# Kernel optimization log

Hardware: AMD Instinct MI355X
Metric: run time of the kernel (lower is better)

Reference implementation:

```python
import jax, jax.numpy as jnp
import numpy as np

B, L, D, H = 2, 2048, 1024, 16
HD = D // H
ROPE_BASE = 10000.0


def _chain_info(lengths):
    """lengths: [B, L] int, chain lengths packed at the front, zeros after.
    Returns per-position within-chain positions (RoPE resets per chain),
    chain ids, and a validity mask."""
    def one(row):
        csum = jnp.cumsum(row)                      # [L]
        total = csum[-1]
        p = jnp.arange(L)
        cid = jnp.searchsorted(csum, p, side='right')  # chain id per position
        prev = jnp.where(cid > 0, csum[jnp.clip(cid - 1, 0, L - 1)], 0)
        valid = p < total
        pos = jnp.where(valid, p - prev, 0).astype(jnp.float32)
        return pos, cid, valid
    return jax.vmap(one)(lengths)


def _rope_tables(pos):
    # pos: [B, L] float -> cos/sin [B, L, 1, HD]
    inv_freq = 1.0 / (ROPE_BASE ** (jnp.arange(0, HD, 2, dtype=jnp.float32) / HD))
    freqs = pos[..., None] * inv_freq               # [B, L, HD/2]
    emb = jnp.concatenate([freqs, freqs], axis=-1)  # [B, L, HD]
    return jnp.cos(emb)[:, :, None, :], jnp.sin(emb)[:, :, None, :]


def _apply_rope(x, cos, sin):
    d = x.shape[-1]
    x1, x2 = x[..., : d // 2], x[..., d // 2:]
    return x * cos + jnp.concatenate([-x2, x1], axis=-1) * sin


def _branch(x, Wqkv, bqkv, cos, sin, allowed):
    # x: [B, L, D]; allowed: [B, L, L] bool attention mask for this branch
    qkv = x @ Wqkv.T + bqkv                          # [B, L, 3D]
    qkv = qkv.reshape(B, L, 3, H, HD)
    q, k, v = qkv[:, :, 0], qkv[:, :, 1], qkv[:, :, 2]
    q = q * (HD ** -0.5)
    q = _apply_rope(q, cos, sin)
    k = _apply_rope(k, cos, sin)
    scores = jnp.einsum('bthd,bshd->bhts', q, k)     # [B, H, L, L]
    scores = jnp.where(allowed[:, None], scores, -jnp.inf)
    probs = jax.nn.softmax(scores, axis=-1)
    probs = jnp.where(jnp.isnan(probs), 0.0, probs)  # fully-masked rows -> 0
    out = jnp.einsum('bhts,bshd->bthd', probs, v)    # [B, L, H, HD]
    return out.reshape(B, L, D)


def setup_inputs() -> dict:
    key = jax.random.key(0)
    ks = jax.random.split(key, 7)
    s = 0.02
    lens = np.zeros((B, L), np.int64)
    lens[0, :8] = [300, 250, 200, 400, 350, 248, 150, 100]   # sum 1998
    lens[1, :6] = [512, 400, 300, 360, 276, 200]             # sum 2048
    return {
        'hidden_states': jax.random.normal(ks[0], (B, L, D), jnp.float32),
        'attention_mask_in_length': jnp.asarray(lens),
        'Wqkv_intra': jax.random.normal(ks[1], (3 * D, D), jnp.float32) * s,
        'bqkv_intra': jnp.zeros((3 * D,), jnp.float32),
        'Wqkv_inter': jax.random.normal(ks[2], (3 * D, D), jnp.float32) * s,
        'bqkv_inter': jnp.zeros((3 * D,), jnp.float32),
        'Wout': jax.random.normal(ks[3], (D, D), jnp.float32) * s,
        'bout': jnp.zeros((D,), jnp.float32),
    }


def reference(hidden_states, attention_mask_in_length, Wqkv_intra, bqkv_intra,
              Wqkv_inter, bqkv_inter, Wout, bout):
    pos, cid, valid = _chain_info(attention_mask_in_length)
    cos, sin = _rope_tables(pos)
    same_chain = cid[:, :, None] == cid[:, None, :]          # [B, L, L]
    key_valid = valid[:, None, :]                            # [B, 1, L]
    allowed_intra = same_chain & key_valid
    allowed_inter = (~same_chain) & key_valid
    out_intra = _branch(hidden_states, Wqkv_intra, bqkv_intra, cos, sin, allowed_intra)
    out_inter = _branch(hidden_states, Wqkv_inter, bqkv_inter, cos, sin, allowed_inter)
    return (out_intra + out_inter) @ Wout.T + bout
```

## Files before the change

kernel.cpp:

```cpp
#include <hip/hip_runtime.h>
#include <hip/hip_bf16.h>
#include <stdint.h>

#define B 2
#define L 2048
#define D 1024
#define H 16
#define HD 64
#define NT (L / 64)
#define NQT (L / 128)
#define INVALID_CID 0x40000000

typedef __hip_bfloat16 bf16;
typedef __attribute__((ext_vector_type(8))) short short8;
typedef __attribute__((ext_vector_type(4))) float floatx4;
typedef __attribute__((ext_vector_type(4))) unsigned int uint4v;

static __device__ __forceinline__ short f2bf(float f) {
    bf16 h = __float2bfloat16(f);
    return *reinterpret_cast<short*>(&h);
}

static __device__ __forceinline__ void async_copy16(const void* g, void* l) {
    __builtin_amdgcn_global_load_lds((__attribute__((address_space(1))) void*)g,
                                     (__attribute__((address_space(3))) void*)l,
                                     16, 0, 0);
}

__global__ void chain_kernel(const int* __restrict__ lens,
                             float* __restrict__ pos, int* __restrict__ cid,
                             int4* __restrict__ tinfo)
{
    __shared__ int csum[L];
    __shared__ int cids[L];
    __shared__ int part[256];
    int b = blockIdx.x;
    int t = threadIdx.x;

    int loc[8];
    int s = 0;
    #pragma unroll
    for (int j = 0; j < 8; ++j) { s += lens[b * L + t * 8 + j]; loc[j] = s; }
    part[t] = s;
    __syncthreads();
    if (t == 0) {
        int acc = 0;
        for (int i = 0; i < 256; ++i) { int v = part[i]; part[i] = acc; acc += v; }
    }
    __syncthreads();
    int base = part[t];
    #pragma unroll
    for (int j = 0; j < 8; ++j) csum[t * 8 + j] = base + loc[j];
    __syncthreads();

    int total = csum[L - 1];
    for (int p = t; p < L; p += 256) {
        int cv;
        if (p < total) {
            int lo = 0, hi = L;
            while (lo < hi) {
                int mid = (lo + hi) >> 1;
                if (csum[mid] <= p) lo = mid + 1; else hi = mid;
            }
            int prev = (lo > 0) ? csum[lo - 1] : 0;
            pos[b * L + p] = (float)(p - prev);
            cv = lo;
        } else {
            pos[b * L + p] = 0.f;
            cv = INVALID_CID;
        }
        cids[p] = cv;
        cid[b * L + p] = cv;
    }
    __syncthreads();
    if (t < NT) {
        int mn = 0x7fffffff, mx = -1, any = 0, all = 1;
        for (int j = 0; j < 64; ++j) {
            int cv = cids[t * 64 + j];
            if (cv != INVALID_CID) { any = 1; mn = min(mn, cv); mx = max(mx, cv); }
            else all = 0;
        }
        tinfo[b * NT + t] = make_int4(mn, mx, any | (all << 1), 0);
    }
}

__global__ void cast_all(const float* __restrict__ x,  const float* __restrict__ Wi,
                         const float* __restrict__ We, const float* __restrict__ Wo,
                         bf16* __restrict__ xb, bf16* __restrict__ Wib,
                         bf16* __restrict__ Web, bf16* __restrict__ Wob)
{
    int bid = blockIdx.x;
    const float* src; bf16* dst; int base;
    if      (bid < 4096)  { src = x;  dst = xb;  base = bid; }
    else if (bid < 7168)  { src = Wi; dst = Wib; base = bid - 4096; }
    else if (bid < 10240) { src = We; dst = Web; base = bid - 7168; }
    else                  { src = Wo; dst = Wob; base = bid - 10240; }
    int i = (base * 256 + threadIdx.x) * 4;
    float4 v = *(const float4*)(src + i);
    dst[i + 0] = __float2bfloat16(v.x);
    dst[i + 1] = __float2bfloat16(v.y);
    dst[i + 2] = __float2bfloat16(v.z);
    dst[i + 3] = __float2bfloat16(v.w);
}

__global__ __launch_bounds__(256, 4) void gemm128(
    const bf16* __restrict__ A, const bf16* __restrict__ Bw,
    const float* __restrict__ bias, const float* __restrict__ bias2,
    void* __restrict__ Cout, int M, int N, int K, int c_bf16, int nsplit)
{
    __shared__ short As[128 * 32];
    __shared__ short Bs[128 * 32];

    int tid = threadIdx.x;
    int wave = tid >> 6, lane = tid & 63;
    int i15 = lane & 15, q8 = lane >> 4;
    int wm = wave & 1, wn = wave >> 1;
    int m0 = blockIdx.y * 128, n0 = blockIdx.x * 128;

    floatx4 acc[4][4];
    #pragma unroll
    for (int mt = 0; mt < 4; ++mt)
        #pragma unroll
        for (int nt = 0; nt < 4; ++nt) acc[mt][nt] = (floatx4){0.f, 0.f, 0.f, 0.f};

    const short* gA = (const short*)A  + (size_t)(m0 + wave * 32 + (lane >> 2)) * K + (lane & 3) * 8;
    const short* gB = (const short*)Bw + (size_t)(n0 + wave * 32 + (lane >> 2)) * K + (lane & 3) * 8;
    short* lA = As + wave * 1024;
    short* lB = Bs + wave * 1024;

    for (int kt = 0; kt < K; kt += 32) {
        __syncthreads();
        async_copy16(gA + kt,          lA);
        async_copy16(gA + 16 * K + kt, lA + 512);
        async_copy16(gB + kt,          lB);
        async_copy16(gB + 16 * K + kt, lB + 512);
        __syncthreads();

        short8 af[4], bfr[4];
        #pragma unroll
        for (int mt = 0; mt < 4; ++mt)
            af[mt] = *(const short8*)&As[(wm * 64 + mt * 16 + i15) * 32 + q8 * 8];
        #pragma unroll
        for (int nt = 0; nt < 4; ++nt)
            bfr[nt] = *(const short8*)&Bs[(wn * 64 + nt * 16 + i15) * 32 + q8 * 8];
        #pragma unroll
        for (int mt = 0; mt < 4; ++mt)
            #pragma unroll
            for (int nt = 0; nt < 4; ++nt)
                acc[mt][nt] = __builtin_amdgcn_mfma_f32_16x16x32_bf16(af[mt], bfr[nt], acc[mt][nt], 0, 0, 0);
    }

    #pragma unroll
    for (int nt = 0; nt < 4; ++nt) {
        int n = n0 + wn * 64 + nt * 16 + i15;
        float bv = (n < nsplit) ? bias[n] : bias2[n - nsplit];
        #pragma unroll
        for (int mt = 0; mt < 4; ++mt) {
            #pragma unroll
            for (int rg = 0; rg < 4; ++rg) {
                int m = m0 + wm * 64 + mt * 16 + q8 * 4 + rg;
                float v = acc[mt][nt][rg] + bv;
                if (c_bf16) ((bf16*)Cout)[(size_t)m * N + n] = __float2bfloat16(v);
                else        ((float*)Cout)[(size_t)m * N + n] = v;
            }
        }
    }
}

__global__ __launch_bounds__(256) void rope_scatter2(
    const bf16* __restrict__ qkv, int rowstride, const float* __restrict__ pos,
    bf16* __restrict__ Qo, bf16* __restrict__ Ko, bf16* __restrict__ Vtg)
{
    __shared__ float Vsh[64][65];
    int tid = threadIdx.x;
    int bid = blockIdx.x;
    int lt = bid & (NT - 1);
    int h  = (bid >> 5) & (H - 1);
    int b  = bid >> 9;
    int l0 = lt * 64;

    const float QSCALE = 0.18033688011111772f;
    int hd = tid & 63, lq = tid >> 6;
    float sgn = (hd < 32) ? -1.f : 1.f;
    float invf = exp2f(-(float)(hd & 31) * (13.287712379549449f / 32.f));

    #pragma unroll
    for (int rr = 0; rr < 16; ++rr) {
        int l = l0 + lq * 16 + rr;
        size_t row = (size_t)(b * L + l) * rowstride;
        int col  = h * HD + hd;
        int col2 = h * HD + (hd ^ 32);

        float xq  = __bfloat162float(qkv[row + col]);
        float xq2 = __bfloat162float(qkv[row + col2]);
        float xk  = __bfloat162float(qkv[row + D + col]);
        float xk2 = __bfloat162float(qkv[row + D + col2]);
        float xv  = __bfloat162float(qkv[row + 2 * D + col]);

        float p = pos[b * L + l];
        float ang = p * invf;
        float cc = cosf(ang), ss = sinf(ang);

        float qo = QSCALE * (xq * cc + sgn * xq2 * ss);
        float ko = xk * cc + sgn * xk2 * ss;

        size_t o = ((size_t)(b * H + h) * L + l) * HD + hd;
        Qo[o] = __float2bfloat16(qo);
        Ko[o] = __float2bfloat16(ko);
        Vsh[l - l0][hd] = xv;
    }
    __syncthreads();
    int lcol = tid & 63, dq = tid >> 6;
    #pragma unroll
    for (int rr = 0; rr < 16; ++rr) {
        int dd = dq * 16 + rr;
        Vtg[((size_t)(b * H + h) * HD + dd) * L + l0 + lcol] = __float2bfloat16(Vsh[lcol][dd]);
    }
}

__global__ __launch_bounds__(256, 2) void attn6(
    const bf16* __restrict__ Q, const bf16* __restrict__ Kg, const bf16* __restrict__ Vtg,
    const int* __restrict__ cid, const int4* __restrict__ tinfo,
    float* __restrict__ OutF, bf16* __restrict__ OutB, const float* __restrict__ Prev,
    int branch)
{
    __shared__ short Ks[2][64][72];
    __shared__ short Vs[2][64][72];
    __shared__ int cls_s[NT];
    __shared__ int list_s[NT];
    __shared__ int nlist_s;

    int tid = threadIdx.x;
    int wave = tid >> 6, lane = tid & 63;
    int i15 = lane & 15, q8 = lane >> 4;
    int workid = ((blockIdx.x & 7) << 6) | (blockIdx.x >> 3);
    int qt = workid & (NQT - 1);
    int h  = (workid >> 4) & (H - 1);
    int b  = workid >> 8;
    int q0 = qt * 128;
    const size_t bh  = (size_t)(b * H + h) * L;
    const size_t bhd = (size_t)(b * H + h) * HD;

    short8 qf[2][2];
    int cq[2];
    #pragma unroll
    for (int g = 0; g < 2; ++g) {
        const short* qp = (const short*)Q + (bh + q0 + g * 64 + wave * 16 + i15) * HD + q8 * 8;
        qf[g][0] = *(const short8*)(qp);
        qf[g][1] = *(const short8*)(qp + 32);
        cq[g] = cid[b * L + q0 + g * 64 + wave * 16 + i15];
    }

    int4 qa = tinfo[b * NT + 2 * qt];
    int4 qb4 = tinfo[b * NT + 2 * qt + 1];
    int4 qinf;
    qinf.x = min(qa.x, qb4.x);
    qinf.y = max(qa.y, qb4.y);
    qinf.z = ((qa.z | qb4.z) & 1) | (qa.z & qb4.z & 2);
    int qall = (qinf.z >> 1) & 1;

    if (tid < NT) {
        int4 ki = tinfo[b * NT + tid];
        int kany = ki.z & 1, kall = (ki.z >> 1) & 1;
        bool disjoint = (ki.x > qinf.y) || (ki.y < qinf.x);
        bool mono = qall && kall && (qinf.x == qinf.y) && (ki.x == ki.y) && (qinf.x == ki.x);
        int cls;
        if (branch == 0) {
            if (!kany || disjoint) cls = 0;
            else if (mono) cls = 2;
            else cls = 1;
        } else {
            if (!kany || mono) cls = 0;
            else if (kall && disjoint) cls = 2;
            else cls = 1;
        }
        cls_s[tid] = cls;
    }
    __syncthreads();
    if (tid == 0) {
        int n = 0;
        for (int t = 0; t < NT; ++t) {
            int c = cls_s[t];
            if (c) list_s[n++] = (t * 64) | ((c == 2) << 16);
        }
        nlist_s = n;
    }
    __syncthreads();
    int n = nlist_s;

    int r = tid >> 2, ccol = (tid & 3) * 16;
    int sr = ((((r >> 2) & 1) | ((r >> 5) << 1)) << 4) | (((r >> 3) & 3) << 2) | (r & 3);
    const short* Kbase = (const short*)Kg  + (bh + r) * HD + ccol;
    const short* Vbase = (const short*)Vtg + (bhd + r) * L + ccol;

    int4 pk0, pk1, pv0, pv1;
    int cur = 0;
    if (n > 0) {
        cur = list_s[0];
        int kt0 = cur & 0xffff;
        pk0 = *(const int4*)(Kbase + (size_t)kt0 * HD);
        pk1 = *(const int4*)(Kbase + (size_t)kt0 * HD + 8);
        pv0 = *(const int4*)(Vbase + kt0);
        pv1 = *(const int4*)(Vbase + kt0 + 8);
    }

    floatx4 accO[2][4];
    #pragma unroll
    for (int g = 0; g < 2; ++g)
        #pragma unroll
        for (int t = 0; t < 4; ++t) accO[g][t] = (floatx4){0.f, 0.f, 0.f, 0.f};
    float lsum[2] = {0.f, 0.f};

    for (int i = 0; i < n; ++i) {
        int kt = cur & 0xffff, full = cur >> 16;
        int buf = i & 1;

        *(int4*)&Ks[buf][sr][ccol]     = pk0;
        *(int4*)&Ks[buf][sr][ccol + 8] = pk1;
        *(int4*)&Vs[buf][r][ccol]      = pv0;
        *(int4*)&Vs[buf][r][ccol + 8]  = pv1;
        __syncthreads();

        if (i + 1 < n) {
            cur = list_s[i + 1];
            int nk = cur & 0xffff;
            pk0 = *(const int4*)(Kbase + (size_t)nk * HD);
            pk1 = *(const int4*)(Kbase + (size_t)nk * HD + 8);
            pv0 = *(const int4*)(Vbase + nk);
            pv1 = *(const int4*)(Vbase + nk + 8);
        }

        unsigned int dl[2][4], dh[2][4];
        #pragma unroll
        for (int t = 0; t < 4; ++t) {
            short8 b0 = *(const short8*)&Ks[buf][t * 16 + i15][q8 * 8];
            short8 b1 = *(const short8*)&Ks[buf][t * 16 + i15][32 + q8 * 8];

            floatx4 accS[2];
            #pragma unroll
            for (int g = 0; g < 2; ++g) {
                accS[g] = (floatx4){0.f, 0.f, 0.f, 0.f};
                accS[g] = __builtin_amdgcn_mfma_f32_16x16x32_bf16(b0, qf[g][0], accS[g], 0, 0, 0);
                accS[g] = __builtin_amdgcn_mfma_f32_16x16x32_bf16(b1, qf[g][1], accS[g], 0, 0, 0);
            }

            if (!full) {
                int4 ck4 = *(const int4*)(cid + b * L + kt + (q8 << 3) + ((t & 1) << 2) + ((t >> 1) << 5));
                int ckr[4] = {ck4.x, ck4.y, ck4.z, ck4.w};
                #pragma unroll
                for (int g = 0; g < 2; ++g)
                    #pragma unroll
                    for (int rg = 0; rg < 4; ++rg) {
                        bool kv = (ckr[rg] != INVALID_CID);
                        bool match = (cq[g] == ckr[rg]);
                        bool ok = kv && (branch ? !match : match);
                        accS[g][rg] = ok ? accS[g][rg] : -1e30f;
                    }
            }

            #pragma unroll
            for (int g = 0; g < 2; ++g) {
                float p0 = __builtin_amdgcn_exp2f(accS[g][0]);
                float p1 = __builtin_amdgcn_exp2f(accS[g][1]);
                float p2 = __builtin_amdgcn_exp2f(accS[g][2]);
                float p3 = __builtin_amdgcn_exp2f(accS[g][3]);
                lsum[g] += (p0 + p1) + (p2 + p3);
                dl[g][t] = (unsigned int)(unsigned short)f2bf(p0) | ((unsigned int)(unsigned short)f2bf(p1) << 16);
                dh[g][t] = (unsigned int)(unsigned short)f2bf(p2) | ((unsigned int)(unsigned short)f2bf(p3) << 16);
            }
        }

        union { uint4v u; short8 s; } pa0[2], pa1[2];
        #pragma unroll
        for (int g = 0; g < 2; ++g) {
            pa0[g].u = (uint4v){dl[g][0], dh[g][0], dl[g][1], dh[g][1]};
            pa1[g].u = (uint4v){dl[g][2], dh[g][2], dl[g][3], dh[g][3]};
        }

        #pragma unroll
        for (int dt = 0; dt < 4; ++dt) {
            short8 vf0 = *(const short8*)&Vs[buf][dt * 16 + i15][q8 * 8];
            short8 vf1 = *(const short8*)&Vs[buf][dt * 16 + i15][32 + q8 * 8];
            #pragma unroll
            for (int g = 0; g < 2; ++g) {
                accO[g][dt] = __builtin_amdgcn_mfma_f32_16x16x32_bf16(pa0[g].s, vf0, accO[g][dt], 0, 0, 0);
                accO[g][dt] = __builtin_amdgcn_mfma_f32_16x16x32_bf16(pa1[g].s, vf1, accO[g][dt], 0, 0, 0);
            }
        }
    }

    #pragma unroll
    for (int g = 0; g < 2; ++g) {
        float ls = lsum[g];
        ls += __shfl_xor(ls, 16, 64);
        ls += __shfl_xor(ls, 32, 64);
        float inv[4];
        #pragma unroll
        for (int rg = 0; rg < 4; ++rg) {
            float lv = __shfl(ls, q8 * 4 + rg, 64);
            inv[rg] = (lv > 0.f) ? 1.f / lv : 0.f;
        }
        #pragma unroll
        for (int t = 0; t < 4; ++t) {
            #pragma unroll
            for (int rg = 0; rg < 4; ++rg) {
                size_t idx = (size_t)(b * L + q0 + g * 64 + wave * 16 + q8 * 4 + rg) * D + h * HD + t * 16 + i15;
                float o = accO[g][t][rg] * inv[rg];
                if (branch == 0) OutF[idx] = o;
                else             OutB[idx] = __float2bfloat16(o + Prev[idx]);
            }
        }
    }
}

extern "C" void kernel_launch(void* const* d_in, const int* in_sizes, int n_in,
                              void* d_out, int out_size, void* d_ws, size_t ws_size,
                              hipStream_t stream)
{
    const float* x    = (const float*)d_in[0];
    const int*   mlen = (const int*)  d_in[1];
    const float* Wi   = (const float*)d_in[2];
    const float* bi   = (const float*)d_in[3];
    const float* We   = (const float*)d_in[4];
    const float* be   = (const float*)d_in[5];
    const float* Wo   = (const float*)d_in[6];
    const float* bo   = (const float*)d_in[7];

    char* ws = (char*)d_ws;
    size_t off = 0;
    auto alloc = [&](size_t bytes) {
        void* p = ws + off;
        off += (bytes + 255) & ~(size_t)255;
        return p;
    };
    bf16*  x_b   = (bf16*) alloc((size_t)B * L * D * 2);
    bf16*  Wi_b  = (bf16*) alloc((size_t)3 * D * D * 2);
    bf16*  We_b  = (bf16*) alloc((size_t)3 * D * D * 2);
    bf16*  Wo_b  = (bf16*) alloc((size_t)D * D * 2);
    bf16*  qkv_b = (bf16*) alloc((size_t)B * L * 6 * D * 2);
    bf16*  q_b   = (bf16*) alloc((size_t)B * H * L * HD * 2);
    bf16*  k_b   = (bf16*) alloc((size_t)B * H * L * HD * 2);
    bf16*  vt_b  = (bf16*) alloc((size_t)B * H * HD * L * 2);
    float* att_i = (float*)alloc((size_t)B * L * D * 4);
    bf16*  sum_b = (bf16*) alloc((size_t)B * L * D * 2);
    float* pos   = (float*)alloc((size_t)B * L * 4);
    int*   cid   = (int*)  alloc((size_t)B * L * 4);
    int4*  tinfo = (int4*) alloc((size_t)B * NT * 16);
    (void)ws_size; (void)n_in; (void)in_sizes; (void)out_size;

    chain_kernel<<<B, 256, 0, stream>>>(mlen, pos, cid, tinfo);

    cast_all<<<11264, 256, 0, stream>>>(x, Wi, We, Wo, x_b, Wi_b, We_b, Wo_b);

    dim3 gq(6 * D / 128, B * L / 128);
    gemm128<<<gq, 256, 0, stream>>>(x_b, Wi_b, bi, be, qkv_b, B * L, 6 * D, D, 1, 3 * D);

    rope_scatter2<<<B * H * NT, 256, 0, stream>>>(qkv_b,         6 * D, pos, q_b, k_b, vt_b);
    attn6<<<B * H * NQT, 256, 0, stream>>>(q_b, k_b, vt_b, cid, tinfo, att_i, sum_b, att_i, 0);

    rope_scatter2<<<B * H * NT, 256, 0, stream>>>(qkv_b + 3 * D, 6 * D, pos, q_b, k_b, vt_b);
    attn6<<<B * H * NQT, 256, 0, stream>>>(q_b, k_b, vt_b, cid, tinfo, att_i, sum_b, att_i, 1);

    dim3 go(D / 128, B * L / 128);
    gemm128<<<go, 256, 0, stream>>>(sum_b, Wo_b, bo, bo, d_out, B * L, D, D, 0, D);
}
```

Baseline: 331.8 us.

## Fuse RoPE and Q/K/V head scatter into the QKV GEMM epilogue

The QKV projection GEMM now applies bias, RoPE (using a precomputed cos/sin table) and the Q scale in its epilogue. It writes Q/K in head-major layout and a transposed V directly for both branches. This removes the intermediate [B,L,6D] bf16 qkv buffer and the two rope_scatter kernel launches, cutting global memory round-trips. The trade-off is a heavier epilogue with scattered stores, extra table reads, and an LDS transpose for V that reuses the GEMM's shared memory after a sync.

```diff
diff --git a/kernel.cpp b/kernel.cpp
--- a/kernel.cpp
+++ b/kernel.cpp
@@ -10,6 +10,7 @@
 #define NT (L / 64)
 #define NQT (L / 128)
 #define INVALID_CID 0x40000000
+#define BHLHD ((size_t)B * H * L * HD)
 
 typedef __hip_bfloat16 bf16;
 typedef __attribute__((ext_vector_type(8))) short short8;
@@ -82,6 +83,15 @@
         }
         tinfo[b * NT + t] = make_int4(mn, mx, any | (all << 1), 0);
     }
+}
+
+__global__ void rope_table(const float* __restrict__ pos, float2* __restrict__ tab)
+{
+    int idx = blockIdx.x * 256 + threadIdx.x;
+    int j = idx & 31, l = idx >> 5;
+    float invf = exp2f(-(float)j * (13.287712379549449f / 32.f));
+    float ang = pos[l] * invf;
+    tab[idx] = make_float2(cosf(ang), sinf(ang));
 }
 
 __global__ void cast_all(const float* __restrict__ x,  const float* __restrict__ Wi,
@@ -103,19 +113,22 @@
     dst[i + 3] = __float2bfloat16(v.w);
 }
 
-__global__ __launch_bounds__(256, 4) void gemm128(
+__global__ __launch_bounds__(256, 4) void gemm_qkv(
     const bf16* __restrict__ A, const bf16* __restrict__ Bw,
-    const float* __restrict__ bias, const float* __restrict__ bias2,
-    void* __restrict__ Cout, int M, int N, int K, int c_bf16, int nsplit)
-{
-    __shared__ short As[128 * 32];
-    __shared__ short Bs[128 * 32];
+    const float* __restrict__ bi, const float* __restrict__ be,
+    const float2* __restrict__ tab,
+    bf16* __restrict__ Qo, bf16* __restrict__ Ko, bf16* __restrict__ Vto)
+{
+    __shared__ short Smem[2 * 128 * 32];
+    short* As = Smem;
+    short* Bs = Smem + 128 * 32;
 
     int tid = threadIdx.x;
     int wave = tid >> 6, lane = tid & 63;
     int i15 = lane & 15, q8 = lane >> 4;
     int wm = wave & 1, wn = wave >> 1;
     int m0 = blockIdx.y * 128, n0 = blockIdx.x * 128;
+    const int K = D;
 
     floatx4 acc[4][4];
     #pragma unroll
@@ -150,10 +163,125 @@
                 acc[mt][nt] = __builtin_amdgcn_mfma_f32_16x16x32_bf16(af[mt], bfr[nt], acc[mt][nt], 0, 0, 0);
     }
 
+    int nb = n0 + wn * 64;
+    int segw = nb >> 10;
+    int br = (segw >= 3);
+    int st = segw - 3 * br;
+    int h = (nb >> 6) & (H - 1);
+    int b = m0 >> 11;
+    int lb = (m0 & (L - 1)) + wm * 64;
+
+    float bv[4];
+    #pragma unroll
+    for (int nt = 0; nt < 4; ++nt) {
+        int n = nb + nt * 16 + i15;
+        bv[nt] = (n < 3 * D) ? bi[n] : be[n - 3 * D];
+    }
+
+    if (st != 2) {
+        bf16* out = (st == 0 ? Qo : Ko) + (size_t)br * BHLHD;
+        const size_t bh = (size_t)(b * H + h) * L;
+        float qs = (st == 0) ? 0.18033688011111772f : 1.0f;
+        #pragma unroll
+        for (int mt = 0; mt < 4; ++mt) {
+            #pragma unroll
+            for (int rg = 0; rg < 4; ++rg) {
+                int m = m0 + wm * 64 + mt * 16 + q8 * 4 + rg;
+                int l = lb + mt * 16 + q8 * 4 + rg;
+                float2 cs0 = tab[(size_t)m * 32 + i15];
+                float2 cs1 = tab[(size_t)m * 32 + 16 + i15];
+                size_t orow = (bh + l) * HD;
+                #pragma unroll
+                for (int nt = 0; nt < 4; ++nt) {
+                    float x  = acc[mt][nt][rg] + bv[nt];
+                    float pr = acc[mt][nt ^ 2][rg] + bv[nt ^ 2];
+                    float cc = (nt & 1) ? cs1.x : cs0.x;
+                    float ss = (nt & 1) ? cs1.y : cs0.y;
+                    float v = qs * (x * cc + ((nt < 2) ? -pr : pr) * ss);
+                    out[orow + nt * 16 + i15] = __float2bfloat16(v);
+                }
+            }
+        }
+    } else {
+        bf16* out = Vto + (size_t)br * BHLHD;
+        const size_t bhd = (size_t)(b * H + h) * HD;
+        __syncthreads();
+        short* vts = Smem + wave * 64 * 20;
+        #pragma unroll
+        for (int mt = 0; mt < 4; ++mt) {
+            #pragma unroll
+            for (int nt = 0; nt < 4; ++nt) {
+                uint2 w;
+                w.x = (unsigned)(unsigned short)f2bf(acc[mt][nt][0] + bv[nt]) |
+                      ((unsigned)(unsigned short)f2bf(acc[mt][nt][1] + bv[nt]) << 16);
+                w.y = (unsigned)(unsigned short)f2bf(acc[mt][nt][2] + bv[nt]) |
+                      ((unsigned)(unsigned short)f2bf(acc[mt][nt][3] + bv[nt]) << 16);
+                *(uint2*)&vts[(nt * 16 + i15) * 20 + q8 * 4] = w;
+            }
+            uint2 r0 = *(const uint2*)&vts[lane * 20 + 0];
+            uint2 r1 = *(const uint2*)&vts[lane * 20 + 4];
+            uint2 r2 = *(const uint2*)&vts[lane * 20 + 8];
+            uint2 r3 = *(const uint2*)&vts[lane * 20 + 12];
+            size_t ga = (bhd + lane) * L + lb + mt * 16;
+            uint4v v0 = (uint4v){r0.x, r0.y, r1.x, r1.y};
+            uint4v v1 = (uint4v){r2.x, r2.y, r3.x, r3.y};
+            *(uint4v*)&out[ga]     = v0;
+            *(uint4v*)&out[ga + 8] = v1;
+        }
+    }
+}
+
+__global__ __launch_bounds__(256, 4) void gemm128(
+    const bf16* __restrict__ A, const bf16* __restrict__ Bw,
+    const float* __restrict__ bias, void* __restrict__ Cout,
+    int M, int N, int K, int c_bf16)
+{
+    __shared__ short As[128 * 32];
+    __shared__ short Bs[128 * 32];
+
+    int tid = threadIdx.x;
+    int wave = tid >> 6, lane = tid & 63;
+    int i15 = lane & 15, q8 = lane >> 4;
+    int wm = wave & 1, wn = wave >> 1;
+    int m0 = blockIdx.y * 128, n0 = blockIdx.x * 128;
+
+    floatx4 acc[4][4];
+    #pragma unroll
+    for (int mt = 0; mt < 4; ++mt)
+        #pragma unroll
+        for (int nt = 0; nt < 4; ++nt) acc[mt][nt] = (floatx4){0.f, 0.f, 0.f, 0.f};
+
+    const short* gA = (const short*)A  + (size_t)(m0 + wave * 32 + (lane >> 2)) * K + (lane & 3) * 8;
+    const short* gB = (const short*)Bw + (size_t)(n0 + wave * 32 + (lane >> 2)) * K + (lane & 3) * 8;
+    short* lA = As + wave * 1024;
+    short* lB = Bs + wave * 1024;
+
+    for (int kt = 0; kt < K; kt += 32) {
+        __syncthreads();
+        async_copy16(gA + kt,          lA);
+        async_copy16(gA + 16 * K + kt, lA + 512);
+        async_copy16(gB + kt,          lB);
+        async_copy16(gB + 16 * K + kt, lB + 512);
+        __syncthreads();
+
+        short8 af[4], bfr[4];
+        #pragma unroll
+        for (int mt = 0; mt < 4; ++mt)
+            af[mt] = *(const short8*)&As[(wm * 64 + mt * 16 + i15) * 32 + q8 * 8];
+        #pragma unroll
+        for (int nt = 0; nt < 4; ++nt)
+            bfr[nt] = *(const short8*)&Bs[(wn * 64 + nt * 16 + i15) * 32 + q8 * 8];
+        #pragma unroll
+        for (int mt = 0; mt < 4; ++mt)
+            #pragma unroll
+            for (int nt = 0; nt < 4; ++nt)
+                acc[mt][nt] = __builtin_amdgcn_mfma_f32_16x16x32_bf16(af[mt], bfr[nt], acc[mt][nt], 0, 0, 0);
+    }
+
     #pragma unroll
     for (int nt = 0; nt < 4; ++nt) {
         int n = n0 + wn * 64 + nt * 16 + i15;
-        float bv = (n < nsplit) ? bias[n] : bias2[n - nsplit];
+        float bv = bias[n];
         #pragma unroll
         for (int mt = 0; mt < 4; ++mt) {
             #pragma unroll
@@ -164,57 +292,6 @@
                 else        ((float*)Cout)[(size_t)m * N + n] = v;
             }
         }
-    }
-}
-
-__global__ __launch_bounds__(256) void rope_scatter2(
-    const bf16* __restrict__ qkv, int rowstride, const float* __restrict__ pos,
-    bf16* __restrict__ Qo, bf16* __restrict__ Ko, bf16* __restrict__ Vtg)
-{
-    __shared__ float Vsh[64][65];
-    int tid = threadIdx.x;
-    int bid = blockIdx.x;
-    int lt = bid & (NT - 1);
-    int h  = (bid >> 5) & (H - 1);
-    int b  = bid >> 9;
-    int l0 = lt * 64;
-
-    const float QSCALE = 0.18033688011111772f;
-    int hd = tid & 63, lq = tid >> 6;
-    float sgn = (hd < 32) ? -1.f : 1.f;
-    float invf = exp2f(-(float)(hd & 31) * (13.287712379549449f / 32.f));
-
-    #pragma unroll
-    for (int rr = 0; rr < 16; ++rr) {
-        int l = l0 + lq * 16 + rr;
-        size_t row = (size_t)(b * L + l) * rowstride;
-        int col  = h * HD + hd;
-        int col2 = h * HD + (hd ^ 32);
-
-        float xq  = __bfloat162float(qkv[row + col]);
-        float xq2 = __bfloat162float(qkv[row + col2]);
-        float xk  = __bfloat162float(qkv[row + D + col]);
-        float xk2 = __bfloat162float(qkv[row + D + col2]);
-        float xv  = __bfloat162float(qkv[row + 2 * D + col]);
-
-        float p = pos[b * L + l];
-        float ang = p * invf;
-        float cc = cosf(ang), ss = sinf(ang);
-
-        float qo = QSCALE * (xq * cc + sgn * xq2 * ss);
-        float ko = xk * cc + sgn * xk2 * ss;
-
-        size_t o = ((size_t)(b * H + h) * L + l) * HD + hd;
-        Qo[o] = __float2bfloat16(qo);
-        Ko[o] = __float2bfloat16(ko);
-        Vsh[l - l0][hd] = xv;
-    }
-    __syncthreads();
-    int lcol = tid & 63, dq = tid >> 6;
-    #pragma unroll
-    for (int rr = 0; rr < 16; ++rr) {
-        int dd = dq * 16 + rr;
-        Vtg[((size_t)(b * H + h) * HD + dd) * L + l0 + lcol] = __float2bfloat16(Vsh[lcol][dd]);
     }
 }
 
@@ -437,30 +514,29 @@
     bf16*  Wi_b  = (bf16*) alloc((size_t)3 * D * D * 2);
     bf16*  We_b  = (bf16*) alloc((size_t)3 * D * D * 2);
     bf16*  Wo_b  = (bf16*) alloc((size_t)D * D * 2);
-    bf16*  qkv_b = (bf16*) alloc((size_t)B * L * 6 * D * 2);
-    bf16*  q_b   = (bf16*) alloc((size_t)B * H * L * HD * 2);
-    bf16*  k_b   = (bf16*) alloc((size_t)B * H * L * HD * 2);
-    bf16*  vt_b  = (bf16*) alloc((size_t)B * H * HD * L * 2);
+    bf16*  q_b   = (bf16*) alloc(2 * BHLHD * 2);
+    bf16*  k_b   = (bf16*) alloc(2 * BHLHD * 2);
+    bf16*  vt_b  = (bf16*) alloc(2 * BHLHD * 2);
     float* att_i = (float*)alloc((size_t)B * L * D * 4);
     bf16*  sum_b = (bf16*) alloc((size_t)B * L * D * 2);
     float* pos   = (float*)alloc((size_t)B * L * 4);
     int*   cid   = (int*)  alloc((size_t)B * L * 4);
     int4*  tinfo = (int4*) alloc((size_t)B * NT * 16);
+    float2* rtab = (float2*)alloc((size_t)B * L * 32 * 8);
     (void)ws_size; (void)n_in; (void)in_sizes; (void)out_size;
 
     chain_kernel<<<B, 256, 0, stream>>>(mlen, pos, cid, tinfo);
+    rope_table<<<B * L * 32 / 256, 256, 0, stream>>>(pos, rtab);
 
     cast_all<<<11264, 256, 0, stream>>>(x, Wi, We, Wo, x_b, Wi_b, We_b, Wo_b);
 
     dim3 gq(6 * D / 128, B * L / 128);
-    gemm128<<<gq, 256, 0, stream>>>(x_b, Wi_b, bi, be, qkv_b, B * L, 6 * D, D, 1, 3 * D);
-
-    rope_scatter2<<<B * H * NT, 256, 0, stream>>>(qkv_b,         6 * D, pos, q_b, k_b, vt_b);
+    gemm_qkv<<<gq, 256, 0, stream>>>(x_b, Wi_b, bi, be, rtab, q_b, k_b, vt_b);
+
     attn6<<<B * H * NQT, 256, 0, stream>>>(q_b, k_b, vt_b, cid, tinfo, att_i, sum_b, att_i, 0);
-
-    rope_scatter2<<<B * H * NT, 256, 0, stream>>>(qkv_b + 3 * D, 6 * D, pos, q_b, k_b, vt_b);
-    attn6<<<B * H * NQT, 256, 0, stream>>>(q_b, k_b, vt_b, cid, tinfo, att_i, sum_b, att_i, 1);
+    attn6<<<B * H * NQT, 256, 0, stream>>>(q_b + BHLHD, k_b + BHLHD, vt_b + BHLHD,
+                                           cid, tinfo, att_i, sum_b, att_i, 1);
 
     dim3 go(D / 128, B * L / 128);
-    gemm128<<<go, 256, 0, stream>>>(sum_b, Wo_b, bo, bo, d_out, B * L, D, D, 0, D);
-}
+    gemm128<<<go, 256, 0, stream>>>(sum_b, Wo_b, bo, d_out, B * L, D, D, 0);
+}
```

After: 306.9 us. 7.5% less time.
